# Optimization experiments

Measured on AMD Instinct MI355X. Metric: run time of the kernel, lower is better.

## Reference

```python
import jax, jax.numpy as jnp
import numpy as np

EPS = 1e-12


def hedgehog_feature_map(W, x):
    # W: [H, D, F], x: [B, H, L, D] -> [B, H, L, 2F]
    o = jnp.einsum('hdf,bhld->bhlf', W, x)
    phi = jnp.concatenate([jax.nn.softmax(o, axis=-1), jax.nn.softmax(-o, axis=-1)], axis=-1)
    return jnp.clip(phi, EPS, None)


def setup_inputs() -> dict:
    key = jax.random.key(0)
    k1, k2, k3, k4, k5 = jax.random.split(key, 5)
    B, H, L, D = 2, 16, 2048, 64
    NFM, F = 4, 64
    q = jax.random.normal(k1, (B, H, L, D), dtype=jnp.float32)
    k = jax.random.normal(k2, (B, H, L, D), dtype=jnp.float32)
    v = jax.random.normal(k3, (B, H, L, D), dtype=jnp.float32)
    # kaiming-uniform-like init for the feature-map projections
    bound = np.sqrt(6.0 / D)
    Wq = jax.random.uniform(k4, (NFM, H, D, F), minval=-bound, maxval=bound, dtype=jnp.float32)
    Wk = jax.random.uniform(k5, (NFM, H, D, F), minval=-bound, maxval=bound, dtype=jnp.float32)
    return {"q": q, "k": k, "v": v, "Wq": Wq, "Wk": Wk, "layer_idx": 0}


def reference(q, k, v, Wq, Wk, layer_idx):
    phi_q = hedgehog_feature_map(Wq[layer_idx], q)  # [B,H,L,2F]
    phi_k = hedgehog_feature_map(Wk[layer_idx], k)  # [B,H,L,2F]
    a = jnp.einsum('bhmf,bhnf->bhmn', phi_q, phi_k)  # [B,H,L,L]
    L = a.shape[-1]
    causal = jnp.tril(jnp.ones((L, L), dtype=bool))  # keep lower-triangular incl. diag
    a = jnp.where(causal, a, 0.0)
    a = a / (jnp.sum(a, axis=-1, keepdims=True) + EPS)
    return jnp.einsum('bhmn,bhnd->bhmd', a, v)
```

## Files before the change

### kernel.cpp

```cpp
#include <hip/hip_runtime.h>

#define BH_N   32
#define H_N    16
#define L_N    2048
#define D_N    64
#define F_N    64
#define FF_N   128
#define CH_N   64
#define NC_N   32
#define EPSF   1e-12f

#define S_STRIDE (D_N*FF_N)
#define SH_TOTAL ((size_t)BH_N*NC_N*S_STRIDE)
#define Z_TOTAL  ((size_t)BH_N*NC_N*FF_N)
#define WT_HEAD  (F_N*D_N)
#define WT_MAT   (H_N*WT_HEAD)

typedef unsigned short u16;
typedef unsigned int   u32;
typedef short bf16x8 __attribute__((ext_vector_type(8)));
typedef float f32x4  __attribute__((ext_vector_type(4)));

#define MFMA16(A,B,C) __builtin_amdgcn_mfma_f32_16x16x32_bf16(A,B,C,0,0,0)

__device__ __forceinline__ void split_hl(float x, u16& h, u16& l){
  unsigned u = __float_as_uint(x);
  h = (u16)(u >> 16);
  float hf = __uint_as_float(u & 0xffff0000u);
  l = (u16)(__float_as_uint(x - hf) >> 16);
}

__device__ __forceinline__ int ix128(int r, int c){ return (r*128 + c) ^ ((r&7)<<3); }
__device__ __forceinline__ int ix64 (int r, int c){ return (r*64  + c) ^ ((r&7)<<3); }
__device__ __forceinline__ int ixA  (int r, int c){ return (r*64  + c) ^ ((r&7)<<2); }

__device__ __forceinline__ bf16x8 ldf128(const u16* t, int r, int k0){
  return *reinterpret_cast<const bf16x8*>(t + ix128(r,k0));
}
__device__ __forceinline__ bf16x8 ldf64(const u16* t, int r, int k0){
  return *reinterpret_cast<const bf16x8*>(t + ix64(r,k0));
}

__device__ __forceinline__ void cvt8(const float* __restrict__ p, bf16x8& h8, bf16x8& l8){
  f32x4 a = *reinterpret_cast<const f32x4*>(p);
  f32x4 b = *reinterpret_cast<const f32x4*>(p+4);
  float v[8] = {a[0],a[1],a[2],a[3],b[0],b[1],b[2],b[3]};
  #pragma unroll
  for (int i=0;i<8;++i){ u16 hh,ll; split_hl(v[i],hh,ll); h8[i]=(short)hh; l8[i]=(short)ll; }
}

__device__ __forceinline__ void o_mfma(const float* __restrict__ X,
                                       const u16* __restrict__ WTh,
                                       const u16* __restrict__ WTl,
                                       int m0, int lane, f32x4 oacc[4])
{
  int lrow = lane&15, k0l = (lane>>4)*8;
  bf16x8 xh[2], xl[2];
  #pragma unroll
  for (int ks=0; ks<2; ++ks)
    cvt8(X + (size_t)(m0+lrow)*D_N + ks*32 + k0l, xh[ks], xl[ks]);
  #pragma unroll
  for (int ft=0; ft<4; ++ft) oacc[ft] = (f32x4){0.f,0.f,0.f,0.f};
  #pragma unroll
  for (int ks=0; ks<2; ++ks){
    #pragma unroll
    for (int ft=0; ft<4; ++ft){
      const u16* bp = WTh + (ft*16+lrow)*D_N + ks*32 + k0l;
      const u16* bq = WTl + (ft*16+lrow)*D_N + ks*32 + k0l;
      bf16x8 wh = *reinterpret_cast<const bf16x8*>(bp);
      bf16x8 wl = *reinterpret_cast<const bf16x8*>(bq);
      oacc[ft] = MFMA16(xh[ks], wh, oacc[ft]);
      oacc[ft] = MFMA16(xh[ks], wl, oacc[ft]);
      oacc[ft] = MFMA16(xl[ks], wh, oacc[ft]);
    }
  }
}

__device__ __forceinline__ void softmax_cl(const f32x4 oacc[4], f32x4 pP[4], f32x4 pM[4])
{
  #pragma unroll
  for (int reg=0; reg<4; ++reg){
    float mP = fmaxf(fmaxf(oacc[0][reg],oacc[1][reg]), fmaxf(oacc[2][reg],oacc[3][reg]));
    float mM = fminf(fminf(oacc[0][reg],oacc[1][reg]), fminf(oacc[2][reg],oacc[3][reg]));
    #pragma unroll
    for (int o=8;o>0;o>>=1){ mP = fmaxf(mP,__shfl_xor(mP,o,64)); mM = fminf(mM,__shfl_xor(mM,o,64)); }
    float eP[4], eM[4], sP=0.f, sM=0.f;
    #pragma unroll
    for (int ft=0; ft<4; ++ft){
      eP[ft] = __expf(oacc[ft][reg]-mP);
      eM[ft] = __expf(mM-oacc[ft][reg]);
      sP += eP[ft]; sM += eM[ft];
    }
    #pragma unroll
    for (int o=8;o>0;o>>=1){ sP += __shfl_xor(sP,o,64); sM += __shfl_xor(sM,o,64); }
    float iP = 1.f/sP, iM = 1.f/sM;
    #pragma unroll
    for (int ft=0; ft<4; ++ft){
      pP[ft][reg] = fmaxf(eP[ft]*iP, EPSF);
      pM[ft][reg] = fmaxf(eM[ft]*iM, EPSF);
    }
  }
}

__device__ __forceinline__ void store_phi_rm(u16* th, u16* tl, int m0, int lane,
                                             const f32x4 pP[4], const f32x4 pM[4]){
  int lrow = lane&15, lkg = lane>>4;
  #pragma unroll
  for (int reg=0; reg<4; ++reg){
    int m = m0 + lkg*4 + reg;
    #pragma unroll
    for (int ft=0; ft<4; ++ft){
      int f = ft*16 + lrow;
      u16 hh,ll;
      split_hl(pP[ft][reg],hh,ll); th[ix128(m,f)]    = hh; tl[ix128(m,f)]    = ll;
      split_hl(pM[ft][reg],hh,ll); th[ix128(m,64+f)] = hh; tl[ix128(m,64+f)] = ll;
    }
  }
}

__device__ __forceinline__ void store_phi_tr(u16* th, u16* tl, int m0, int lane,
                                             const f32x4 pP[4], const f32x4 pM[4]){
  int lrow = lane&15, lkg = lane>>4;
  #pragma unroll
  for (int reg=0; reg<4; ++reg){
    int m = m0 + lkg*4 + reg;
    #pragma unroll
    for (int ft=0; ft<4; ++ft){
      int f = ft*16 + lrow;
      u16 hh,ll;
      split_hl(pP[ft][reg],hh,ll); th[ix64(f,m)]    = hh; tl[ix64(f,m)]    = ll;
      split_hl(pM[ft][reg],hh,ll); th[ix64(64+f,m)] = hh; tl[ix64(64+f,m)] = ll;
    }
  }
}

__global__ __launch_bounds__(256)
void hh_wprep(const float* __restrict__ Wq, const float* __restrict__ Wk,
              const int* __restrict__ lidx, u16* __restrict__ WT)
{
  __shared__ float tile[64*65];
  int bid = blockIdx.x, which = bid & 1, h = bid >> 1;
  const float* Wsrc = (which ? Wk : Wq) + (size_t)(*lidx)*(H_N*D_N*F_N) + (size_t)h*(D_N*F_N);
  u16* dh = WT + which*(2*WT_MAT) + h*WT_HEAD;
  u16* dl = dh + WT_MAT;
  int t = threadIdx.x;
  #pragma unroll
  for (int i=0;i<16;++i){
    int idx = i*256 + t;
    tile[(idx&63)*65 + (idx>>6)] = Wsrc[idx];
  }
  __syncthreads();
  #pragma unroll
  for (int i=0;i<16;++i){
    int idx = i*256 + t;
    float w = tile[(idx>>6)*65 + (idx&63)];
    u16 hh,ll; split_hl(w,hh,ll);
    dh[idx] = hh; dl[idx] = ll;
  }
}

__global__ __launch_bounds__(256,3)
void hh_chunksums(const float* __restrict__ kin, const float* __restrict__ vin,
                  const u16* __restrict__ WkT,
                  u16* __restrict__ Sh_ws, u16* __restrict__ Sl_ws,
                  float* __restrict__ z_ws)
{
  __shared__ __align__(16) char sm[51200];
  u16*  pkT_h = (u16*)sm;
  u16*  pkT_l = (u16*)(sm + 16384);
  u16*  vt_h  = (u16*)(sm + 32768);
  u16*  vt_l  = (u16*)(sm + 40960);
  float* zb   = (float*)(sm + 49152);

  int bid = blockIdx.x, bh = bid>>5, c = bid & (NC_N-1), h = bh & (H_N-1);
  const float* Xk = kin + ((size_t)bh*L_N + c*CH_N)*D_N;
  const float* Vc = vin + ((size_t)bh*L_N + c*CH_N)*D_N;
  const u16* Wh = WkT + h*WT_HEAD;
  const u16* Wl = Wh + WT_MAT;
  int t = threadIdx.x, lane = t&63, w = t>>6;

  int vn = t>>2, vd0 = (t&3)*16;
  float4 vreg[4];
  #pragma unroll
  for (int p=0;p<4;++p)
    vreg[p] = *reinterpret_cast<const float4*>(Vc + (size_t)vn*D_N + vd0 + p*4);

  f32x4 oacc[4], pP[4], pM[4];
  o_mfma(Xk, Wh, Wl, w*16, lane, oacc);
  softmax_cl(oacc, pP, pM);
  store_phi_tr(pkT_h, pkT_l, w*16, lane, pP, pM);

  #pragma unroll
  for (int ft=0; ft<4; ++ft){
    float sP = pP[ft][0]+pP[ft][1]+pP[ft][2]+pP[ft][3];
    float sM = pM[ft][0]+pM[ft][1]+pM[ft][2]+pM[ft][3];
    sP += __shfl_xor(sP,16,64); sP += __shfl_xor(sP,32,64);
    sM += __shfl_xor(sM,16,64); sM += __shfl_xor(sM,32,64);
    if ((lane>>4)==0){
      zb[w*128 + ft*16 + lane]      = sP;
      zb[w*128 + 64 + ft*16 + lane] = sM;
    }
  }

  #pragma unroll
  for (int p=0;p<4;++p){
    float vals[4] = {vreg[p].x, vreg[p].y, vreg[p].z, vreg[p].w};
    #pragma unroll
    for (int e=0;e<4;++e){
      int d = vd0 + p*4 + e;
      u16 hh,ll; split_hl(vals[e],hh,ll);
      vt_h[ix64(d, vn)] = hh;
      vt_l[ix64(d, vn)] = ll;
    }
  }
  __syncthreads();

  if (t < FF_N)
    z_ws[(size_t)(bh*NC_N + c)*FF_N + t] = zb[t] + zb[128+t] + zb[256+t] + zb[384+t];

  int m0 = w*16, lrow = lane&15, k0l = (lane>>4)*8;
  f32x4 acc[8];
  #pragma unroll
  for (int ft=0; ft<8; ++ft) acc[ft] = (f32x4){0.f,0.f,0.f,0.f};
  #pragma unroll
  for (int ks=0; ks<2; ++ks){
    int r0k = ks*32 + k0l;
    bf16x8 ah = ldf64(vt_h, m0 + lrow, r0k);
    bf16x8 al = ldf64(vt_l, m0 + lrow, r0k);
    #pragma unroll
    for (int ft=0; ft<8; ++ft){
      bf16x8 bh = ldf64(pkT_h, ft*16 + lrow, r0k);
      bf16x8 bl = ldf64(pkT_l, ft*16 + lrow, r0k);
      acc[ft] = MFMA16(ah, bh, acc[ft]);
      acc[ft] = MFMA16(ah, bl, acc[ft]);
      acc[ft] = MFMA16(al, bh, acc[ft]);
    }
  }
  u16* Shout = Sh_ws + (size_t)(bh*NC_N + c)*S_STRIDE;
  u16* Slout = Sl_ws + (size_t)(bh*NC_N + c)*S_STRIDE;
  #pragma unroll
  for (int ft=0; ft<8; ++ft)
    #pragma unroll
    for (int reg=0; reg<4; ++reg){
      int d = m0 + (lane>>4)*4 + reg;
      int idx = d*FF_N + ft*16 + lrow;
      u16 hh,ll; split_hl(acc[ft][reg],hh,ll);
      Shout[idx] = hh; Slout[idx] = ll;
    }
}

__global__ __launch_bounds__(256)
void hh_scan(u16* __restrict__ Sh_ws, u16* __restrict__ Sl_ws,
             float* __restrict__ z_ws)
{
  int bid = blockIdx.x;
  int bh = bid / 17, s = bid % 17;
  int t = threadIdx.x;
  if (s < 16){
    size_t base = (size_t)bh*NC_N*S_STRIDE + (size_t)s*512 + 2*t;
    float run0 = 0.f, run1 = 0.f;
    u32 nh = *reinterpret_cast<const u32*>(Sh_ws + base);
    u32 nl = *reinterpret_cast<const u32*>(Sl_ws + base);
    #pragma unroll
    for (int c=0; c<NC_N; ++c){
      u32 ch = nh, cl = nl;
      if (c+1 < NC_N){
        nh = *reinterpret_cast<const u32*>(Sh_ws + base + (size_t)(c+1)*S_STRIDE);
        nl = *reinterpret_cast<const u32*>(Sl_ws + base + (size_t)(c+1)*S_STRIDE);
      }
      u16 h0,l0,h1,l1; split_hl(run0,h0,l0); split_hl(run1,h1,l1);
      *reinterpret_cast<u32*>(Sh_ws + base + (size_t)c*S_STRIDE) = (u32)h0 | ((u32)h1<<16);
      *reinterpret_cast<u32*>(Sl_ws + base + (size_t)c*S_STRIDE) = (u32)l0 | ((u32)l1<<16);
      run0 += __uint_as_float((ch & 0xffffu) << 16) + __uint_as_float((cl & 0xffffu) << 16);
      run1 += __uint_as_float(ch & 0xffff0000u)     + __uint_as_float(cl & 0xffff0000u);
    }
  } else if (t < FF_N){
    size_t base = (size_t)bh*NC_N*FF_N + t;
    float run = 0.f;
    float nxt = z_ws[base];
    #pragma unroll
    for (int c=0;c<NC_N;++c){
      float cur = nxt;
      if (c+1 < NC_N) nxt = z_ws[base + (size_t)(c+1)*FF_N];
      z_ws[base + (size_t)c*FF_N] = run;
      run += cur;
    }
  }
}

__global__ __launch_bounds__(256,3)
void hh_output(const float* __restrict__ qin, const float* __restrict__ kin,
               const float* __restrict__ vin,
               const u16* __restrict__ WT,
               const u16* __restrict__ Sh_ws, const u16* __restrict__ Sl_ws,
               const float* __restrict__ z_ws,
               float* __restrict__ out)
{
  __shared__ __align__(16) char sm[32768];
  u16*  ph   = (u16*)sm;
  u16*  pl   = (u16*)(sm + 16384);
  float* aA  = (float*)sm;
  u16*  vt_h = (u16*)(sm + 16384);
  u16*  vt_l = (u16*)(sm + 24576);

  int bid = blockIdx.x, bh = bid>>5, c = bid & (NC_N-1), h = bh & (H_N-1);
  const float* Xq = qin + ((size_t)bh*L_N + c*CH_N)*D_N;
  const float* Xk = kin + ((size_t)bh*L_N + c*CH_N)*D_N;
  const float* Vc = vin + ((size_t)bh*L_N + c*CH_N)*D_N;
  const u16* Sph = Sh_ws + (size_t)(bh*NC_N + c)*S_STRIDE;
  const u16* Spl = Sl_ws + (size_t)(bh*NC_N + c)*S_STRIDE;
  const float* zp = z_ws + (size_t)(bh*NC_N + c)*FF_N;
  const u16* WqTh = WT + h*WT_HEAD;
  const u16* WqTl = WqTh + WT_MAT;
  const u16* WkTh = WT + 2*WT_MAT + h*WT_HEAD;
  const u16* WkTl = WkTh + WT_MAT;
  int t = threadIdx.x, lane = t&63, w = t>>6;
  int m0 = w*16, lrow = lane&15, lkg = lane>>4, k0l = lkg*8;

  f32x4 oacc[4], pP[4], pM[4];
  o_mfma(Xq, WqTh, WqTl, m0, lane, oacc);
  softmax_cl(oacc, pP, pM);

  float dz[4];
  {
    float zqP[4], zqM[4];
    #pragma unroll
    for (int ft=0; ft<4; ++ft){
      zqP[ft] = zp[ft*16 + lrow];
      zqM[ft] = zp[64 + ft*16 + lrow];
    }
    #pragma unroll
    for (int reg=0; reg<4; ++reg){
      float s = 0.f;
      #pragma unroll
      for (int ft=0; ft<4; ++ft)
        s += pP[ft][reg]*zqP[ft] + pM[ft][reg]*zqM[ft];
      #pragma unroll
      for (int o=8;o>0;o>>=1) s += __shfl_xor(s,o,64);
      dz[reg] = s;
    }
  }

  store_phi_rm(ph, pl, m0, lane, pP, pM);
  bf16x8 qh[4], ql[4];
  #pragma unroll
  for (int ks=0; ks<4; ++ks){
    qh[ks] = ldf128(ph, m0 + lrow, ks*32 + k0l);
    ql[ks] = ldf128(pl, m0 + lrow, ks*32 + k0l);
  }

  f32x4 accA[4], accO[4];
  #pragma unroll
  for (int i=0;i<4;++i){ accA[i]=(f32x4){0,0,0,0}; accO[i]=(f32x4){0,0,0,0}; }
  #pragma unroll
  for (int ks=0; ks<4; ++ks){
    int f0 = ks*32 + k0l;
    #pragma unroll
    for (int dt=0; dt<4; ++dt){
      bf16x8 sh = *reinterpret_cast<const bf16x8*>(Sph + (size_t)(dt*16 + lrow)*FF_N + f0);
      bf16x8 sl = *reinterpret_cast<const bf16x8*>(Spl + (size_t)(dt*16 + lrow)*FF_N + f0);
      accO[dt] = MFMA16(qh[ks], sh, accO[dt]);
      accO[dt] = MFMA16(qh[ks], sl, accO[dt]);
      accO[dt] = MFMA16(ql[ks], sh, accO[dt]);
    }
  }

  o_mfma(Xk, WkTh, WkTl, m0, lane, oacc);
  softmax_cl(oacc, pP, pM);
  store_phi_rm(ph, pl, m0, lane, pP, pM);

  int vn = t>>2, vd0 = (t&3)*16;
  float4 vreg[4];
  #pragma unroll
  for (int p=0;p<4;++p)
    vreg[p] = *reinterpret_cast<const float4*>(Vc + (size_t)vn*D_N + vd0 + p*4);

  __syncthreads();

  #pragma unroll
  for (int ks=0; ks<4; ++ks){
    int f0 = ks*32 + k0l;
    #pragma unroll
    for (int nt=0; nt<4; ++nt){
      if (nt <= w){
        bf16x8 kh = ldf128(ph, nt*16 + lrow, f0);
        bf16x8 kl = ldf128(pl, nt*16 + lrow, f0);
        accA[nt] = MFMA16(qh[ks], kh, accA[nt]);
        accA[nt] = MFMA16(qh[ks], kl, accA[nt]);
        accA[nt] = MFMA16(ql[ks], kh, accA[nt]);
      }
    }
  }

  float rs[4] = {0.f,0.f,0.f,0.f};
  #pragma unroll
  for (int nt=0; nt<4; ++nt)
    #pragma unroll
    for (int reg=0; reg<4; ++reg){
      float a = accA[nt][reg];
      if (nt > w) a = 0.f;
      if (nt == w && lrow > lkg*4 + reg) a = 0.f;
      accA[nt][reg] = a;
      rs[reg] += a;
    }
  float den[4];
  #pragma unroll
  for (int reg=0; reg<4; ++reg){
    float s = rs[reg];
    s += __shfl_xor(s,1,64); s += __shfl_xor(s,2,64);
    s += __shfl_xor(s,4,64); s += __shfl_xor(s,8,64);
    den[reg] = dz[reg] + s + EPSF;
  }

  __syncthreads();

  #pragma unroll
  for (int nt=0; nt<4; ++nt)
    #pragma unroll
    for (int reg=0; reg<4; ++reg){
      int m = m0 + lkg*4 + reg;
      aA[ixA(m, nt*16 + lrow)] = accA[nt][reg];
    }
  #pragma unroll
  for (int p=0;p<4;++p){
    float vals[4] = {vreg[p].x, vreg[p].y, vreg[p].z, vreg[p].w};
    #pragma unroll
    for (int e=0;e<4;++e){
      int d = vd0 + p*4 + e;
      u16 hh,ll; split_hl(vals[e],hh,ll);
      vt_h[ix64(d, vn)] = hh;
      vt_l[ix64(d, vn)] = ll;
    }
  }
  __syncthreads();

  #pragma unroll
  for (int ks=0; ks<2; ++ks){
    if (ks <= (w>>1)){
      int n0 = ks*32 + k0l;
      int m  = m0 + lrow;
      f32x4 a0 = *reinterpret_cast<const f32x4*>(aA + ixA(m, n0));
      f32x4 a1 = *reinterpret_cast<const f32x4*>(aA + ixA(m, n0+4));
      float av[8] = {a0[0],a0[1],a0[2],a0[3],a1[0],a1[1],a1[2],a1[3]};
      bf16x8 Ah, Al;
      #pragma unroll
      for (int i=0;i<8;++i){ u16 hh,ll; split_hl(av[i],hh,ll); Ah[i]=(short)hh; Al[i]=(short)ll; }
      #pragma unroll
      for (int dt=0; dt<4; ++dt){
        bf16x8 vh = ldf64(vt_h, dt*16 + lrow, n0);
        bf16x8 vl = ldf64(vt_l, dt*16 + lrow, n0);
        accO[dt] = MFMA16(Ah, vh, accO[dt]);
        accO[dt] = MFMA16(Ah, vl, accO[dt]);
        accO[dt] = MFMA16(Al, vh, accO[dt]);
      }
    }
  }

  #pragma unroll
  for (int reg=0; reg<4; ++reg){
    float inv = 1.0f / den[reg];
    int m = m0 + lkg*4 + reg;
    float* orow = out + ((size_t)bh*L_N + c*CH_N + m)*D_N;
    #pragma unroll
    for (int dt=0; dt<4; ++dt)
      orow[dt*16 + lrow] = accO[dt][reg] * inv;
  }
}

extern "C" void kernel_launch(void* const* d_in, const int* in_sizes, int n_in,
                              void* d_out, int out_size, void* d_ws, size_t ws_size,
                              hipStream_t stream) {
  const float* q    = (const float*)d_in[0];
  const float* k    = (const float*)d_in[1];
  const float* v    = (const float*)d_in[2];
  const float* Wq   = (const float*)d_in[3];
  const float* Wk   = (const float*)d_in[4];
  const int*   lidx = (const int*)d_in[5];
  float* out  = (float*)d_out;
  u16*   Sh_ws = (u16*)d_ws;
  u16*   Sl_ws = Sh_ws + SH_TOTAL;
  float* z_ws  = (float*)(Sl_ws + SH_TOTAL);
  u16*   WT    = (u16*)(z_ws + Z_TOTAL);

  hh_wprep    <<<2*H_N,     256, 0, stream>>>(Wq, Wk, lidx, WT);
  hh_chunksums<<<BH_N*NC_N, 256, 0, stream>>>(k, v, WT + 2*WT_MAT, Sh_ws, Sl_ws, z_ws);
  hh_scan     <<<BH_N*17,   256, 0, stream>>>(Sh_ws, Sl_ws, z_ws);
  hh_output   <<<BH_N*NC_N, 256, 0, stream>>>(q, k, v, WT, Sh_ws, Sl_ws, z_ws, out);
}
```

Before: 187.4 us.

## Load V directly into MFMA fragments and raise occupancy in chunk kernels

In the chunk-sum kernel, each lane now loads V columns straight from global memory and splits them into bf16 hi/lo MFMA operands in registers. This removes the transposed V staging in shared memory and cuts LDS use from 51200 to 34816 bytes. Both the chunk-sum and output kernels raise the launch-bounds occupancy hint from 3 to 4 blocks. In the output kernel, the inter-chunk state MFMA loop is moved after the barrier and interleaved with the intra-chunk attention MFMAs, which shortens accumulator live ranges. The per-lane strided V loads are less coalesced, and the tighter register budget could cause spills.

Measured after the change: 159.7 us. 14.8% less time.

```diff
diff --git a/kernel.cpp b/kernel.cpp
--- a/kernel.cpp
+++ b/kernel.cpp
@@ -159,18 +159,16 @@
   }
 }
 
-__global__ __launch_bounds__(256,3)
+__global__ __launch_bounds__(256,4)
 void hh_chunksums(const float* __restrict__ kin, const float* __restrict__ vin,
                   const u16* __restrict__ WkT,
                   u16* __restrict__ Sh_ws, u16* __restrict__ Sl_ws,
                   float* __restrict__ z_ws)
 {
-  __shared__ __align__(16) char sm[51200];
+  __shared__ __align__(16) char sm[34816];
   u16*  pkT_h = (u16*)sm;
   u16*  pkT_l = (u16*)(sm + 16384);
-  u16*  vt_h  = (u16*)(sm + 32768);
-  u16*  vt_l  = (u16*)(sm + 40960);
-  float* zb   = (float*)(sm + 49152);
+  float* zb   = (float*)(sm + 32768);
 
   int bid = blockIdx.x, bh = bid>>5, c = bid & (NC_N-1), h = bh & (H_N-1);
   const float* Xk = kin + ((size_t)bh*L_N + c*CH_N)*D_N;
@@ -178,17 +176,19 @@
   const u16* Wh = WkT + h*WT_HEAD;
   const u16* Wl = Wh + WT_MAT;
   int t = threadIdx.x, lane = t&63, w = t>>6;
-
-  int vn = t>>2, vd0 = (t&3)*16;
-  float4 vreg[4];
-  #pragma unroll
-  for (int p=0;p<4;++p)
-    vreg[p] = *reinterpret_cast<const float4*>(Vc + (size_t)vn*D_N + vd0 + p*4);
+  int m0 = w*16, lrow = lane&15, k0l = (lane>>4)*8;
+
+  float vcol[16];
+  #pragma unroll
+  for (int ks=0; ks<2; ++ks)
+    #pragma unroll
+    for (int j=0; j<8; ++j)
+      vcol[ks*8+j] = Vc[(size_t)(ks*32 + k0l + j)*D_N + m0 + lrow];
 
   f32x4 oacc[4], pP[4], pM[4];
-  o_mfma(Xk, Wh, Wl, w*16, lane, oacc);
+  o_mfma(Xk, Wh, Wl, m0, lane, oacc);
   softmax_cl(oacc, pP, pM);
-  store_phi_tr(pkT_h, pkT_l, w*16, lane, pP, pM);
+  store_phi_tr(pkT_h, pkT_l, m0, lane, pP, pM);
 
   #pragma unroll
   for (int ft=0; ft<4; ++ft){
@@ -201,39 +201,33 @@
       zb[w*128 + 64 + ft*16 + lane] = sM;
     }
   }
-
-  #pragma unroll
-  for (int p=0;p<4;++p){
-    float vals[4] = {vreg[p].x, vreg[p].y, vreg[p].z, vreg[p].w};
-    #pragma unroll
-    for (int e=0;e<4;++e){
-      int d = vd0 + p*4 + e;
-      u16 hh,ll; split_hl(vals[e],hh,ll);
-      vt_h[ix64(d, vn)] = hh;
-      vt_l[ix64(d, vn)] = ll;
-    }
-  }
   __syncthreads();
 
   if (t < FF_N)
     z_ws[(size_t)(bh*NC_N + c)*FF_N + t] = zb[t] + zb[128+t] + zb[256+t] + zb[384+t];
 
-  int m0 = w*16, lrow = lane&15, k0l = (lane>>4)*8;
+  bf16x8 ah[2], al[2];
+  #pragma unroll
+  for (int ks=0; ks<2; ++ks)
+    #pragma unroll
+    for (int j=0; j<8; ++j){
+      u16 hh,ll; split_hl(vcol[ks*8+j],hh,ll);
+      ah[ks][j]=(short)hh; al[ks][j]=(short)ll;
+    }
+
   f32x4 acc[8];
   #pragma unroll
   for (int ft=0; ft<8; ++ft) acc[ft] = (f32x4){0.f,0.f,0.f,0.f};
   #pragma unroll
   for (int ks=0; ks<2; ++ks){
     int r0k = ks*32 + k0l;
-    bf16x8 ah = ldf64(vt_h, m0 + lrow, r0k);
-    bf16x8 al = ldf64(vt_l, m0 + lrow, r0k);
     #pragma unroll
     for (int ft=0; ft<8; ++ft){
       bf16x8 bh = ldf64(pkT_h, ft*16 + lrow, r0k);
       bf16x8 bl = ldf64(pkT_l, ft*16 + lrow, r0k);
-      acc[ft] = MFMA16(ah, bh, acc[ft]);
-      acc[ft] = MFMA16(ah, bl, acc[ft]);
-      acc[ft] = MFMA16(al, bh, acc[ft]);
+      acc[ft] = MFMA16(ah[ks], bh, acc[ft]);
+      acc[ft] = MFMA16(ah[ks], bl, acc[ft]);
+      acc[ft] = MFMA16(al[ks], bh, acc[ft]);
     }
   }
   u16* Shout = Sh_ws + (size_t)(bh*NC_N + c)*S_STRIDE;
@@ -288,7 +282,7 @@
   }
 }
 
-__global__ __launch_bounds__(256,3)
+__global__ __launch_bounds__(256,4)
 void hh_output(const float* __restrict__ qin, const float* __restrict__ kin,
                const float* __restrict__ vin,
                const u16* __restrict__ WT,
@@ -349,22 +343,6 @@
     ql[ks] = ldf128(pl, m0 + lrow, ks*32 + k0l);
   }
 
-  f32x4 accA[4], accO[4];
-  #pragma unroll
-  for (int i=0;i<4;++i){ accA[i]=(f32x4){0,0,0,0}; accO[i]=(f32x4){0,0,0,0}; }
-  #pragma unroll
-  for (int ks=0; ks<4; ++ks){
-    int f0 = ks*32 + k0l;
-    #pragma unroll
-    for (int dt=0; dt<4; ++dt){
-      bf16x8 sh = *reinterpret_cast<const bf16x8*>(Sph + (size_t)(dt*16 + lrow)*FF_N + f0);
-      bf16x8 sl = *reinterpret_cast<const bf16x8*>(Spl + (size_t)(dt*16 + lrow)*FF_N + f0);
-      accO[dt] = MFMA16(qh[ks], sh, accO[dt]);
-      accO[dt] = MFMA16(qh[ks], sl, accO[dt]);
-      accO[dt] = MFMA16(ql[ks], sh, accO[dt]);
-    }
-  }
-
   o_mfma(Xk, WkTh, WkTl, m0, lane, oacc);
   softmax_cl(oacc, pP, pM);
   store_phi_rm(ph, pl, m0, lane, pP, pM);
@@ -376,6 +354,10 @@
     vreg[p] = *reinterpret_cast<const float4*>(Vc + (size_t)vn*D_N + vd0 + p*4);
 
   __syncthreads();
+
+  f32x4 accA[4], accO[4];
+  #pragma unroll
+  for (int i=0;i<4;++i){ accA[i]=(f32x4){0,0,0,0}; accO[i]=(f32x4){0,0,0,0}; }
 
   #pragma unroll
   for (int ks=0; ks<4; ++ks){
@@ -389,6 +371,14 @@
         accA[nt] = MFMA16(qh[ks], kl, accA[nt]);
         accA[nt] = MFMA16(ql[ks], kh, accA[nt]);
       }
+    }
+    #pragma unroll
+    for (int dt=0; dt<4; ++dt){
+      bf16x8 sh = *reinterpret_cast<const bf16x8*>(Sph + (size_t)(dt*16 + lrow)*FF_N + f0);
+      bf16x8 sl = *reinterpret_cast<const bf16x8*>(Spl + (size_t)(dt*16 + lrow)*FF_N + f0);
+      accO[dt] = MFMA16(qh[ks], sh, accO[dt]);
+      accO[dt] = MFMA16(qh[ks], sl, accO[dt]);
+      accO[dt] = MFMA16(ql[ks], sh, accO[dt]);
     }
   }
 
```
